# Kernel tuning notes

Measured on AMD Instinct MI355X. Metric: run time of the kernel, lower is better.

Reference implementation:

```python
import jax, jax.numpy as jnp
import numpy as np

HIDDEN = 1024
VOCAB = 50257
MAXLEN = 64


def setup_inputs() -> dict:
    key = jax.random.key(0)
    ks = jax.random.split(key, 16)
    s = 0.02
    return {
        "token": jax.random.randint(ks[0], (1,), 0, VOCAB, dtype=jnp.int64),
        "hidden": jax.random.normal(ks[1], (1, 1, HIDDEN), dtype=jnp.float32),
        "encoder_outputs": jax.random.normal(ks[2], (MAXLEN, HIDDEN), dtype=jnp.float32),
        "emb": jax.random.normal(ks[3], (VOCAB, HIDDEN), dtype=jnp.float32) * s,
        "attn_W": jax.random.normal(ks[4], (MAXLEN, 2 * HIDDEN), dtype=jnp.float32) * s,
        "attn_b": jnp.zeros((MAXLEN,), dtype=jnp.float32),
        "comb_W": jax.random.normal(ks[5], (HIDDEN, 2 * HIDDEN), dtype=jnp.float32) * s,
        "comb_b": jnp.zeros((HIDDEN,), dtype=jnp.float32),
        "W_ih": jax.random.normal(ks[6], (3 * HIDDEN, HIDDEN), dtype=jnp.float32) * s,
        "W_hh": jax.random.normal(ks[7], (3 * HIDDEN, HIDDEN), dtype=jnp.float32) * s,
        "b_ih": jnp.zeros((3 * HIDDEN,), dtype=jnp.float32),
        "b_hh": jnp.zeros((3 * HIDDEN,), dtype=jnp.float32),
        "out_W": jax.random.normal(ks[8], (VOCAB, HIDDEN), dtype=jnp.float32) * s,
        "out_b": jnp.zeros((VOCAB,), dtype=jnp.float32),
    }


def reference(token, hidden, encoder_outputs, emb, attn_W, attn_b,
              comb_W, comb_b, W_ih, W_hh, b_ih, b_hh, out_W, out_b):
    # embedded: [1, H] (dropout is identity in eval mode)
    embedded = emb[token].reshape(1, -1)
    h0 = hidden[0]  # [1, H]
    # attention over the encoder window: [1, MAXLEN]
    scores = jnp.concatenate([embedded, h0], axis=1) @ attn_W.T + attn_b
    attn_weights = jax.nn.softmax(scores, axis=1)
    # context: [1, H]
    attn_applied = attn_weights @ encoder_outputs
    # combine + relu: [1, H]
    x = jnp.concatenate([embedded, attn_applied], axis=1) @ comb_W.T + comb_b
    x = jax.nn.relu(x)
    # single GRU step (PyTorch gate math)
    gi = x @ W_ih.T + b_ih    # [1, 3H]
    gh = h0 @ W_hh.T + b_hh   # [1, 3H]
    i_r, i_z, i_n = jnp.split(gi, 3, axis=1)
    h_r, h_z, h_n = jnp.split(gh, 3, axis=1)
    r = jax.nn.sigmoid(i_r + h_r)
    z = jax.nn.sigmoid(i_z + h_z)
    n = jnp.tanh(i_n + r * h_n)
    h_new = (1.0 - z) * n + z * h0  # [1, H]
    logits = h_new @ out_W.T + out_b  # [1, VOCAB]
    return logits, h_new[None, :, :], attn_weights
```

## Files before the change

kernel.cpp:

```cpp
#include <hip/hip_runtime.h>
#include <math.h>

#define HIDDEN 1024
#define VOCAB  50257
#define MAXLEN 64

__device__ __forceinline__ float wave_reduce_sum(float v) {
    #pragma unroll
    for (int off = 32; off > 0; off >>= 1)
        v += __shfl_down(v, off, 64);
    return v;
}

__global__ void k_scores(const int* __restrict__ token,
                         const float* __restrict__ emb,
                         const float* __restrict__ hidden,
                         const float* __restrict__ attn_W,
                         const float* __restrict__ attn_b,
                         float* __restrict__ ws_scores) {
    const int m = blockIdx.x;
    const int t = threadIdx.x;
    const float* erow = emb + (size_t)token[0] * HIDDEN;
    const float4* Wrow = (const float4*)(attn_W + (size_t)m * 2 * HIDDEN);
    float acc = 0.f;
    #pragma unroll
    for (int it = 0; it < 2; ++it) {
        int i = t + it * 256;
        float4 w4 = Wrow[i];
        int k = i * 4;
        const float* src = (k < HIDDEN) ? (erow + k) : (hidden + k - HIDDEN);
        float4 c4 = *(const float4*)src;
        acc += w4.x * c4.x + w4.y * c4.y + w4.z * c4.z + w4.w * c4.w;
    }
    __shared__ float part[4];
    acc = wave_reduce_sum(acc);
    const int wid = t >> 6, lane = t & 63;
    if (lane == 0) part[wid] = acc;
    __syncthreads();
    if (t == 0)
        ws_scores[m] = part[0] + part[1] + part[2] + part[3] + attn_b[m];
}

__global__ void k_softmax(const float* __restrict__ ws_scores,
                          float* __restrict__ ws_w,
                          float* __restrict__ out_attn) {
    const int l = threadIdx.x;
    float s = ws_scores[l];
    float m = s;
    #pragma unroll
    for (int off = 32; off > 0; off >>= 1) m = fmaxf(m, __shfl_xor(m, off, 64));
    float e = expf(s - m);
    float sum = e;
    #pragma unroll
    for (int off = 32; off > 0; off >>= 1) sum += __shfl_xor(sum, off, 64);
    float w = e / sum;
    ws_w[l] = w;
    out_attn[l] = w;
}

__global__ void k_context(const float* __restrict__ ws_w,
                          const float* __restrict__ enc,
                          float* __restrict__ ws_ctx) {
    __shared__ float w[MAXLEN];
    const int t = threadIdx.x;
    if (t < MAXLEN) w[t] = ws_w[t];
    __syncthreads();
    const int h = blockIdx.x * 256 + t;
    float acc = 0.f;
    #pragma unroll 8
    for (int m = 0; m < MAXLEN; ++m)
        acc += w[m] * enc[(size_t)m * HIDDEN + h];
    ws_ctx[h] = acc;
}

__global__ void k_combine(const int* __restrict__ token,
                          const float* __restrict__ emb,
                          const float* __restrict__ ws_ctx,
                          const float* __restrict__ comb_W,
                          const float* __restrict__ comb_b,
                          float* __restrict__ ws_x) {
    const int wid = threadIdx.x >> 6, lane = threadIdx.x & 63;
    const int j = blockIdx.x * 4 + wid;
    const float* erow = emb + (size_t)token[0] * HIDDEN;
    const float4* Wrow = (const float4*)(comb_W + (size_t)j * 2 * HIDDEN);
    float acc = 0.f;
    #pragma unroll
    for (int it = 0; it < 8; ++it) {
        int i = lane + it * 64;
        float4 w4 = Wrow[i];
        int k = i * 4;
        const float* src = (k < HIDDEN) ? (erow + k) : (ws_ctx + k - HIDDEN);
        float4 c4 = *(const float4*)src;
        acc += w4.x * c4.x + w4.y * c4.y + w4.z * c4.z + w4.w * c4.w;
    }
    acc = wave_reduce_sum(acc);
    if (lane == 0) ws_x[j] = fmaxf(acc + comb_b[j], 0.f);
}

__global__ void k_gru(const float* __restrict__ ws_x,
                      const float* __restrict__ hidden,
                      const float* __restrict__ W_ih,
                      const float* __restrict__ W_hh,
                      const float* __restrict__ b_ih,
                      const float* __restrict__ b_hh,
                      float* __restrict__ ws_h,
                      float* __restrict__ out_h) {
    const int wid = threadIdx.x >> 6, lane = threadIdx.x & 63;
    const int j = blockIdx.x * 4 + wid;
    float d[6];
    const float* rows[6] = {
        W_ih + (size_t)j * HIDDEN,
        W_ih + (size_t)(j + HIDDEN) * HIDDEN,
        W_ih + (size_t)(j + 2 * HIDDEN) * HIDDEN,
        W_hh + (size_t)j * HIDDEN,
        W_hh + (size_t)(j + HIDDEN) * HIDDEN,
        W_hh + (size_t)(j + 2 * HIDDEN) * HIDDEN };
    const float* vecs[2] = { ws_x, hidden };
    #pragma unroll
    for (int q = 0; q < 6; ++q) {
        const float4* W4 = (const float4*)rows[q];
        const float4* v4 = (const float4*)vecs[q / 3];
        float acc = 0.f;
        #pragma unroll
        for (int it = 0; it < 4; ++it) {
            int i = lane + it * 64;
            float4 a = W4[i];
            float4 b = v4[i];
            acc += a.x * b.x + a.y * b.y + a.z * b.z + a.w * b.w;
        }
        d[q] = wave_reduce_sum(acc);
    }
    if (lane == 0) {
        float i_r = d[0] + b_ih[j];
        float i_z = d[1] + b_ih[j + HIDDEN];
        float i_n = d[2] + b_ih[j + 2 * HIDDEN];
        float h_r = d[3] + b_hh[j];
        float h_z = d[4] + b_hh[j + HIDDEN];
        float h_n = d[5] + b_hh[j + 2 * HIDDEN];
        float r = 1.f / (1.f + expf(-(i_r + h_r)));
        float z = 1.f / (1.f + expf(-(i_z + h_z)));
        float n = tanhf(i_n + r * h_n);
        float h0v = hidden[j];
        float hn = (1.f - z) * n + z * h0v;
        ws_h[j] = hn;
        out_h[j] = hn;
    }
}

__global__ void k_logits(const float* __restrict__ ws_h,
                         const float* __restrict__ out_W,
                         const float* __restrict__ out_b,
                         float* __restrict__ out_logits) {
    __shared__ float4 hn[HIDDEN / 4];
    const int t = threadIdx.x;
    hn[t] = ((const float4*)ws_h)[t];
    __syncthreads();
    const int wid = t >> 6, lane = t & 63;
    const int v = blockIdx.x * 4 + wid;
    if (v >= VOCAB) return;
    const float4* Wrow = (const float4*)(out_W + (size_t)v * HIDDEN);
    float acc = 0.f;
    #pragma unroll
    for (int i = 0; i < 4; ++i) {
        float4 a = Wrow[lane + i * 64];
        float4 b = hn[lane + i * 64];
        acc += a.x * b.x + a.y * b.y + a.z * b.z + a.w * b.w;
    }
    acc = wave_reduce_sum(acc);
    if (lane == 0) out_logits[v] = acc + out_b[v];
}

extern "C" void kernel_launch(void* const* d_in, const int* in_sizes, int n_in,
                              void* d_out, int out_size, void* d_ws, size_t ws_size,
                              hipStream_t stream) {
    const int*   token  = (const int*)d_in[0];
    const float* hidden = (const float*)d_in[1];
    const float* enc    = (const float*)d_in[2];
    const float* emb    = (const float*)d_in[3];
    const float* attn_W = (const float*)d_in[4];
    const float* attn_b = (const float*)d_in[5];
    const float* comb_W = (const float*)d_in[6];
    const float* comb_b = (const float*)d_in[7];
    const float* W_ih   = (const float*)d_in[8];
    const float* W_hh   = (const float*)d_in[9];
    const float* b_ih   = (const float*)d_in[10];
    const float* b_hh   = (const float*)d_in[11];
    const float* out_W  = (const float*)d_in[12];
    const float* out_b  = (const float*)d_in[13];

    float* out = (float*)d_out;
    float* out_logits = out;
    float* out_h      = out + VOCAB;
    float* out_attn   = out + VOCAB + HIDDEN;

    float* ws = (float*)d_ws;
    float* ws_scores = ws;
    float* ws_w      = ws + 64;
    float* ws_ctx    = ws + 128;
    float* ws_x      = ws + 1152;
    float* ws_h      = ws + 2176;

    k_scores<<<MAXLEN, 256, 0, stream>>>(token, emb, hidden, attn_W, attn_b, ws_scores);
    k_softmax<<<1, 64, 0, stream>>>(ws_scores, ws_w, out_attn);
    k_context<<<HIDDEN / 256, 256, 0, stream>>>(ws_w, enc, ws_ctx);
    k_combine<<<HIDDEN / 4, 256, 0, stream>>>(token, emb, ws_ctx, comb_W, comb_b, ws_x);
    k_gru<<<HIDDEN / 4, 256, 0, stream>>>(ws_x, hidden, W_ih, W_hh, b_ih, b_hh, ws_h, out_h);
    k_logits<<<(VOCAB + 3) / 4, 256, 0, stream>>>(ws_h, out_W, out_b, out_logits);
}
```

Measured before the change: 55.88 us.

## Fuse attention, softmax, context and combine into one redundant per-block kernel

Merges the scores, softmax, context and combine kernels into a single kernel, k_pre. Each of the 256 blocks recomputes the full attention scores, softmax and context vector in shared memory, then computes its own four rows of the combine projection. This removes three kernel launches and their serialization gaps, at the cost of every block re-reading attn_W (512KB) and encoder_outputs (256KB), relying on L2 to absorb the repeated reads. Separately, the logits kernel now has each wave compute two vocabulary rows, which halves the grid size and gives each wave more loads in flight.

```diff
diff --git a/kernel.cpp b/kernel.cpp
--- a/kernel.cpp
+++ b/kernel.cpp
@@ -12,99 +12,107 @@
     return v;
 }
 
-__global__ void k_scores(const int* __restrict__ token,
-                         const float* __restrict__ emb,
-                         const float* __restrict__ hidden,
-                         const float* __restrict__ attn_W,
-                         const float* __restrict__ attn_b,
-                         float* __restrict__ ws_scores) {
-    const int m = blockIdx.x;
+__global__ __launch_bounds__(256) void k_pre(
+    const int* __restrict__ token,
+    const float* __restrict__ emb,
+    const float* __restrict__ hidden,
+    const float* __restrict__ enc,
+    const float* __restrict__ attn_W,
+    const float* __restrict__ attn_b,
+    const float* __restrict__ comb_W,
+    const float* __restrict__ comb_b,
+    float* __restrict__ ws_x,
+    float* __restrict__ out_attn)
+{
+    __shared__ float cvec[2 * HIDDEN];
+    __shared__ float sc[MAXLEN];
+    __shared__ float wsm[MAXLEN];
+
     const int t = threadIdx.x;
+    const int wid = t >> 6, lane = t & 63;
     const float* erow = emb + (size_t)token[0] * HIDDEN;
-    const float4* Wrow = (const float4*)(attn_W + (size_t)m * 2 * HIDDEN);
-    float acc = 0.f;
-    #pragma unroll
-    for (int it = 0; it < 2; ++it) {
-        int i = t + it * 256;
-        float4 w4 = Wrow[i];
-        int k = i * 4;
-        const float* src = (k < HIDDEN) ? (erow + k) : (hidden + k - HIDDEN);
-        float4 c4 = *(const float4*)src;
-        acc += w4.x * c4.x + w4.y * c4.y + w4.z * c4.z + w4.w * c4.w;
-    }
-    __shared__ float part[4];
-    acc = wave_reduce_sum(acc);
-    const int wid = t >> 6, lane = t & 63;
-    if (lane == 0) part[wid] = acc;
-    __syncthreads();
-    if (t == 0)
-        ws_scores[m] = part[0] + part[1] + part[2] + part[3] + attn_b[m];
-}
-
-__global__ void k_softmax(const float* __restrict__ ws_scores,
-                          float* __restrict__ ws_w,
-                          float* __restrict__ out_attn) {
-    const int l = threadIdx.x;
-    float s = ws_scores[l];
-    float m = s;
-    #pragma unroll
-    for (int off = 32; off > 0; off >>= 1) m = fmaxf(m, __shfl_xor(m, off, 64));
-    float e = expf(s - m);
-    float sum = e;
-    #pragma unroll
-    for (int off = 32; off > 0; off >>= 1) sum += __shfl_xor(sum, off, 64);
-    float w = e / sum;
-    ws_w[l] = w;
-    out_attn[l] = w;
-}
-
-__global__ void k_context(const float* __restrict__ ws_w,
-                          const float* __restrict__ enc,
-                          float* __restrict__ ws_ctx) {
-    __shared__ float w[MAXLEN];
-    const int t = threadIdx.x;
-    if (t < MAXLEN) w[t] = ws_w[t];
-    __syncthreads();
-    const int h = blockIdx.x * 256 + t;
-    float acc = 0.f;
-    #pragma unroll 8
-    for (int m = 0; m < MAXLEN; ++m)
-        acc += w[m] * enc[(size_t)m * HIDDEN + h];
-    ws_ctx[h] = acc;
-}
-
-__global__ void k_combine(const int* __restrict__ token,
-                          const float* __restrict__ emb,
-                          const float* __restrict__ ws_ctx,
-                          const float* __restrict__ comb_W,
-                          const float* __restrict__ comb_b,
-                          float* __restrict__ ws_x) {
-    const int wid = threadIdx.x >> 6, lane = threadIdx.x & 63;
-    const int j = blockIdx.x * 4 + wid;
-    const float* erow = emb + (size_t)token[0] * HIDDEN;
-    const float4* Wrow = (const float4*)(comb_W + (size_t)j * 2 * HIDDEN);
-    float acc = 0.f;
-    #pragma unroll
-    for (int it = 0; it < 8; ++it) {
-        int i = lane + it * 64;
-        float4 w4 = Wrow[i];
-        int k = i * 4;
-        const float* src = (k < HIDDEN) ? (erow + k) : (ws_ctx + k - HIDDEN);
-        float4 c4 = *(const float4*)src;
-        acc += w4.x * c4.x + w4.y * c4.y + w4.z * c4.z + w4.w * c4.w;
-    }
-    acc = wave_reduce_sum(acc);
-    if (lane == 0) ws_x[j] = fmaxf(acc + comb_b[j], 0.f);
-}
-
-__global__ void k_gru(const float* __restrict__ ws_x,
-                      const float* __restrict__ hidden,
-                      const float* __restrict__ W_ih,
-                      const float* __restrict__ W_hh,
-                      const float* __restrict__ b_ih,
-                      const float* __restrict__ b_hh,
-                      float* __restrict__ ws_h,
-                      float* __restrict__ out_h) {
+
+    {
+        float4* cv4 = (float4*)cvec;
+        cv4[t]       = ((const float4*)erow)[t];
+        cv4[t + 256] = ((const float4*)hidden)[t];
+    }
+    __syncthreads();
+
+    for (int m = wid; m < MAXLEN; m += 4) {
+        const float4* Wr  = (const float4*)(attn_W + (size_t)m * 2 * HIDDEN);
+        const float4* cv4 = (const float4*)cvec;
+        float acc = 0.f;
+        #pragma unroll
+        for (int it = 0; it < 8; ++it) {
+            int i = lane + it * 64;
+            float4 a = Wr[i]; float4 b = cv4[i];
+            acc += a.x * b.x + a.y * b.y + a.z * b.z + a.w * b.w;
+        }
+        acc = wave_reduce_sum(acc);
+        if (lane == 0) sc[m] = acc + attn_b[m];
+    }
+    __syncthreads();
+
+    if (wid == 0) {
+        float s = sc[lane];
+        float mx = s;
+        #pragma unroll
+        for (int off = 32; off > 0; off >>= 1) mx = fmaxf(mx, __shfl_xor(mx, off, 64));
+        float e = expf(s - mx);
+        float sum = e;
+        #pragma unroll
+        for (int off = 32; off > 0; off >>= 1) sum += __shfl_xor(sum, off, 64);
+        float wv = e / sum;
+        wsm[lane] = wv;
+        if (blockIdx.x == 0) out_attn[lane] = wv;
+    }
+    __syncthreads();
+
+    {
+        float a0 = 0.f, a1 = 0.f, a2 = 0.f, a3 = 0.f;
+        #pragma unroll 4
+        for (int m = 0; m < MAXLEN; ++m) {
+            float wv = wsm[m];
+            const float* er = enc + (size_t)m * HIDDEN;
+            a0 += wv * er[t];
+            a1 += wv * er[t + 256];
+            a2 += wv * er[t + 512];
+            a3 += wv * er[t + 768];
+        }
+        cvec[HIDDEN + t]       = a0;
+        cvec[HIDDEN + t + 256] = a1;
+        cvec[HIDDEN + t + 512] = a2;
+        cvec[HIDDEN + t + 768] = a3;
+    }
+    __syncthreads();
+
+    {
+        const int j = blockIdx.x * 4 + wid;
+        const float4* Wr  = (const float4*)(comb_W + (size_t)j * 2 * HIDDEN);
+        const float4* cv4 = (const float4*)cvec;
+        float acc = 0.f;
+        #pragma unroll
+        for (int it = 0; it < 8; ++it) {
+            int i = lane + it * 64;
+            float4 a = Wr[i]; float4 b = cv4[i];
+            acc += a.x * b.x + a.y * b.y + a.z * b.z + a.w * b.w;
+        }
+        acc = wave_reduce_sum(acc);
+        if (lane == 0) ws_x[j] = fmaxf(acc + comb_b[j], 0.f);
+    }
+}
+
+__global__ __launch_bounds__(256) void k_gru(
+    const float* __restrict__ ws_x,
+    const float* __restrict__ hidden,
+    const float* __restrict__ W_ih,
+    const float* __restrict__ W_hh,
+    const float* __restrict__ b_ih,
+    const float* __restrict__ b_hh,
+    float* __restrict__ ws_h,
+    float* __restrict__ out_h)
+{
     const int wid = threadIdx.x >> 6, lane = threadIdx.x & 63;
     const int j = blockIdx.x * 4 + wid;
     float d[6];
@@ -147,27 +155,41 @@
     }
 }
 
-__global__ void k_logits(const float* __restrict__ ws_h,
-                         const float* __restrict__ out_W,
-                         const float* __restrict__ out_b,
-                         float* __restrict__ out_logits) {
+__global__ __launch_bounds__(256) void k_logits(
+    const float* __restrict__ ws_h,
+    const float* __restrict__ out_W,
+    const float* __restrict__ out_b,
+    float* __restrict__ out_logits)
+{
     __shared__ float4 hn[HIDDEN / 4];
     const int t = threadIdx.x;
     hn[t] = ((const float4*)ws_h)[t];
     __syncthreads();
     const int wid = t >> 6, lane = t & 63;
-    const int v = blockIdx.x * 4 + wid;
-    if (v >= VOCAB) return;
-    const float4* Wrow = (const float4*)(out_W + (size_t)v * HIDDEN);
-    float acc = 0.f;
+    const int v0 = blockIdx.x * 8 + wid * 2;
+    const int v1 = v0 + 1;
+    if (v0 >= VOCAB) return;
+    const float4* W0 = (const float4*)(out_W + (size_t)v0 * HIDDEN);
+    const float4* W1 = (const float4*)(out_W + (size_t)v1 * HIDDEN);
+    const bool has1 = (v1 < VOCAB);
+    float acc0 = 0.f, acc1 = 0.f;
     #pragma unroll
     for (int i = 0; i < 4; ++i) {
-        float4 a = Wrow[lane + i * 64];
-        float4 b = hn[lane + i * 64];
-        acc += a.x * b.x + a.y * b.y + a.z * b.z + a.w * b.w;
-    }
-    acc = wave_reduce_sum(acc);
-    if (lane == 0) out_logits[v] = acc + out_b[v];
+        const int idx = lane + i * 64;
+        float4 b = hn[idx];
+        float4 a0 = W0[idx];
+        acc0 += a0.x * b.x + a0.y * b.y + a0.z * b.z + a0.w * b.w;
+        if (has1) {
+            float4 a1 = W1[idx];
+            acc1 += a1.x * b.x + a1.y * b.y + a1.z * b.z + a1.w * b.w;
+        }
+    }
+    acc0 = wave_reduce_sum(acc0);
+    acc1 = wave_reduce_sum(acc1);
+    if (lane == 0) {
+        out_logits[v0] = acc0 + out_b[v0];
+        if (has1) out_logits[v1] = acc1 + out_b[v1];
+    }
 }
 
 extern "C" void kernel_launch(void* const* d_in, const int* in_sizes, int n_in,
@@ -194,16 +216,11 @@
     float* out_attn   = out + VOCAB + HIDDEN;
 
     float* ws = (float*)d_ws;
-    float* ws_scores = ws;
-    float* ws_w      = ws + 64;
-    float* ws_ctx    = ws + 128;
-    float* ws_x      = ws + 1152;
-    float* ws_h      = ws + 2176;
-
-    k_scores<<<MAXLEN, 256, 0, stream>>>(token, emb, hidden, attn_W, attn_b, ws_scores);
-    k_softmax<<<1, 64, 0, stream>>>(ws_scores, ws_w, out_attn);
-    k_context<<<HIDDEN / 256, 256, 0, stream>>>(ws_w, enc, ws_ctx);
-    k_combine<<<HIDDEN / 4, 256, 0, stream>>>(token, emb, ws_ctx, comb_W, comb_b, ws_x);
+    float* ws_x = ws;
+    float* ws_h = ws + 1024;
+
+    k_pre<<<HIDDEN / 4, 256, 0, stream>>>(token, emb, hidden, enc, attn_W, attn_b,
+                                          comb_W, comb_b, ws_x, out_attn);
     k_gru<<<HIDDEN / 4, 256, 0, stream>>>(ws_x, hidden, W_ih, W_hh, b_ih, b_hh, ws_h, out_h);
-    k_logits<<<(VOCAB + 3) / 4, 256, 0, stream>>>(ws_h, out_W, out_b, out_logits);
-}
+    k_logits<<<(VOCAB + 7) / 8, 256, 0, stream>>>(ws_h, out_W, out_b, out_logits);
+}
```

Result: slower. 86.21 us (+54.3%).
